# Kernel tuning notes

Measured on AMD Instinct MI355X. Metric: run time of the kernel, lower is better.

The kernel has to match this reference:

```python
import jax, jax.numpy as jnp
import numpy as np

B, T, D, K, P = 32, 512, 80, 16, 64
LAMBDA_MU = 0.1
LAMBDA_L = 0.1
N_SUBJECTS = float(P)


def _make_chol(key, prefix, d):
    # Valid lower-triangular Cholesky factors with positive diagonal.
    a = jax.random.normal(key, prefix + (d, d), dtype=jnp.float32) * 0.05
    strict = jnp.tril(a, -1)
    diag = 0.5 + jax.nn.softplus(jnp.einsum('...ii->...i', a))
    return strict + diag[..., None] * jnp.eye(d, dtype=jnp.float32)


def setup_inputs() -> dict:
    key = jax.random.key(0)
    k = jax.random.split(key, 7)
    x = jax.random.normal(k[0], (B, T, D), dtype=jnp.float32)
    g = jax.random.uniform(k[1], (B, T, K), dtype=jnp.float32)
    gamma = g / jnp.sum(g, axis=-1, keepdims=True)  # responsibilities sum to 1
    mu_pop = jax.random.normal(k[2], (K, D), dtype=jnp.float32) * 0.5
    mu_subj = mu_pop[None] + jax.random.normal(k[3], (P, K, D), dtype=jnp.float32) * 0.1
    L_pop = _make_chol(k[4], (K,), D)
    L_subj = _make_chol(k[5], (P, K), D)
    subject_ids = jax.random.randint(k[6], (B,), 0, P, dtype=jnp.int32)
    return dict(x=x, mu_pop=mu_pop, L_pop=L_pop, mu_subj=mu_subj,
                L_subj=L_subj, gamma=gamma, subject_ids=subject_ids)


def reference(x, mu_pop, L_pop, mu_subj, L_subj, gamma, subject_ids):
    dtype = mu_pop.dtype
    Bx, Tx, Dx = x.shape
    Pn = mu_subj.shape[0]
    # Gather subject parameters per batch row (equivalent to the TF
    # sort-by-subject + ragged per-block loop, vectorized).
    mu_b = mu_subj[subject_ids]   # (B,K,D)
    L_b = L_subj[subject_ids]     # (B,K,D,D)
    r = x[:, :, None, :] - mu_b[:, None, :, :]   # (B,T,K,D)
    rT = jnp.transpose(r, (0, 2, 3, 1))          # (B,K,D,T)
    y = jax.lax.linalg.triangular_solve(L_b, rT, left_side=True, lower=True)  # (B,K,D,T)
    mahal = jnp.sum(y * y, axis=2)               # (B,K,T)
    logdet = 2.0 * jnp.sum(jnp.log(jnp.diagonal(L_b, axis1=-2, axis2=-1)), axis=-1)  # (B,K)
    log2pi = jnp.asarray(np.log(2.0 * np.pi), dtype)
    logp = -0.5 * (Dx * log2pi + logdet[:, :, None] + mahal)  # (B,K,T)
    nll = -jnp.sum(jnp.transpose(gamma, (0, 2, 1)) * logp) / (Bx * Tx)
    # Regularization over subjects present in the batch.
    mask = jnp.zeros((Pn,), dtype).at[subject_ids].set(1.0)
    S = jnp.sum(mask)
    mu_reg = jnp.sum(mask[:, None, None] * jnp.square(mu_subj - mu_pop[None]))
    L_reg = jnp.sum(mask[:, None, None, None] * jnp.square(L_subj - L_pop[None]))
    scale = S / N_SUBJECTS
    return nll + scale * (LAMBDA_MU / 2.0 * mu_reg + LAMBDA_L / 2.0 * L_reg)
```

## Files before the change

kernel.cpp:

```cpp
#include <hip/hip_runtime.h>

#define NB 32
#define NT 512
#define ND 80
#define NK 16
#define NP 64

#define C_DLOG2PI (80.0f * 1.837877066409345f)

#define REG_CHUNKS 16

__global__ void zero_out_kernel(float* out) { out[0] = 0.0f; }

__global__ __launch_bounds__(512) void nll_kernel(
    const float* __restrict__ x,
    const float* __restrict__ mu_subj,
    const float* __restrict__ L_subj,
    const float* __restrict__ gamma,
    const int* __restrict__ sids,
    float* __restrict__ out)
{
    const int bk  = blockIdx.x;
    const int b   = bk / NK;
    const int k   = bk % NK;
    const int tid = threadIdx.x;
    const int s   = sids[b];

    __shared__ float Ls[ND * ND];
    __shared__ float mus[ND];
    __shared__ float invd[ND];
    __shared__ float logd[ND];
    __shared__ float logdet_sh;
    __shared__ float partial[8];

    const float* Lg = L_subj + (((size_t)s * NK + k) * ND * ND);
    for (int i = tid; i < ND * ND; i += 512) Ls[i] = Lg[i];
    const float* mg = mu_subj + (((size_t)s * NK + k) * ND);
    if (tid < ND) mus[tid] = mg[tid];
    __syncthreads();

    if (tid < ND) {
        float dg = Ls[tid * ND + tid];
        invd[tid] = 1.0f / dg;
        logd[tid] = logf(dg);
    }
    __syncthreads();
    if (tid == 0) {
        float sum = 0.0f;
        for (int i = 0; i < ND; ++i) sum += logd[i];
        logdet_sh = 2.0f * sum;
    }
    __syncthreads();
    const float logdet = logdet_sh;

    const int t = tid;
    const float* xp = x + (((size_t)b * NT + t) * ND);
    float r[ND];
    #pragma unroll
    for (int i4 = 0; i4 < ND / 4; ++i4) {
        float4 v = reinterpret_cast<const float4*>(xp)[i4];
        r[4 * i4 + 0] = v.x - mus[4 * i4 + 0];
        r[4 * i4 + 1] = v.y - mus[4 * i4 + 1];
        r[4 * i4 + 2] = v.z - mus[4 * i4 + 2];
        r[4 * i4 + 3] = v.w - mus[4 * i4 + 3];
    }

    float mahal = 0.0f;
    #pragma unroll
    for (int i = 0; i < ND; ++i) {
        float acc = r[i];
        #pragma unroll
        for (int j = 0; j < i; ++j) acc -= Ls[i * ND + j] * r[j];
        float yi = acc * invd[i];
        r[i] = yi;
        mahal += yi * yi;
    }

    float logp = -0.5f * (C_DLOG2PI + logdet + mahal);
    float g = gamma[(((size_t)b * NT + t) * NK) + k];
    float local = g * logp;

    #pragma unroll
    for (int off = 32; off > 0; off >>= 1) local += __shfl_down(local, off);
    int wave = tid >> 6;
    if ((tid & 63) == 0) partial[wave] = local;
    __syncthreads();
    if (tid == 0) {
        float sum = 0.0f;
        #pragma unroll
        for (int w = 0; w < 8; ++w) sum += partial[w];
        atomicAdd(out, -sum * (1.0f / (NB * NT)));
    }
}

__global__ __launch_bounds__(256) void reg_kernel(
    const float* __restrict__ mu_pop,
    const float* __restrict__ L_pop,
    const float* __restrict__ mu_subj,
    const float* __restrict__ L_subj,
    const int* __restrict__ sids,
    float* __restrict__ out)
{
    const int p   = blockIdx.y;
    const int c   = blockIdx.x;
    const int tid = threadIdx.x;

    __shared__ float scale_sh;
    __shared__ int   present_sh;
    __shared__ float partial[4];

    if (tid == 0) {
        unsigned long long seen = 0ull;
        int present = 0;
        for (int b = 0; b < NB; ++b) {
            int sb = sids[b];
            seen |= (1ull << sb);
            present |= (sb == p) ? 1 : 0;
        }
        present_sh = present;
        scale_sh = (float)__popcll(seen) * (1.0f / (float)NP);
    }
    __syncthreads();
    if (!present_sh) return;

    float acc = 0.0f;

    {
        const float4* Ls4 = reinterpret_cast<const float4*>(L_subj + (size_t)p * NK * ND * ND);
        const float4* Lp4 = reinterpret_cast<const float4*>(L_pop);
        const int n4 = NK * ND * ND / 4;
        for (int i = c * 256 + tid; i < n4; i += REG_CHUNKS * 256) {
            float4 a = Ls4[i];
            float4 bq = Lp4[i];
            float dx = a.x - bq.x, dy = a.y - bq.y, dz = a.z - bq.z, dw = a.w - bq.w;
            acc += dx * dx + dy * dy + dz * dz + dw * dw;
        }
    }
    if (c == 0) {
        const float4* ms4 = reinterpret_cast<const float4*>(mu_subj + (size_t)p * NK * ND);
        const float4* mp4 = reinterpret_cast<const float4*>(mu_pop);
        const int n4 = NK * ND / 4;
        for (int i = tid; i < n4; i += 256) {
            float4 a = ms4[i];
            float4 bq = mp4[i];
            float dx = a.x - bq.x, dy = a.y - bq.y, dz = a.z - bq.z, dw = a.w - bq.w;
            acc += dx * dx + dy * dy + dz * dz + dw * dw;
        }
    }

    #pragma unroll
    for (int off = 32; off > 0; off >>= 1) acc += __shfl_down(acc, off);
    int wave = tid >> 6;
    if ((tid & 63) == 0) partial[wave] = acc;
    __syncthreads();
    if (tid == 0) {
        float total = partial[0] + partial[1] + partial[2] + partial[3];
        atomicAdd(out, scale_sh * 0.05f * total);
    }
}

extern "C" void kernel_launch(void* const* d_in, const int* in_sizes, int n_in,
                              void* d_out, int out_size, void* d_ws, size_t ws_size,
                              hipStream_t stream) {
    (void)in_sizes; (void)n_in; (void)d_ws; (void)ws_size; (void)out_size;
    const float* x       = (const float*)d_in[0];
    const float* mu_pop  = (const float*)d_in[1];
    const float* L_pop   = (const float*)d_in[2];
    const float* mu_subj = (const float*)d_in[3];
    const float* L_subj  = (const float*)d_in[4];
    const float* gamma   = (const float*)d_in[5];
    const int*   sids    = (const int*)d_in[6];
    float* out = (float*)d_out;

    hipLaunchKernelGGL(zero_out_kernel, dim3(1), dim3(1), 0, stream, out);
    hipLaunchKernelGGL(nll_kernel, dim3(NB * NK), dim3(512), 0, stream,
                       x, mu_subj, L_subj, gamma, sids, out);
    hipLaunchKernelGGL(reg_kernel, dim3(REG_CHUNKS, NP), dim3(256), 0, stream,
                       mu_pop, L_pop, mu_subj, L_subj, sids, out);
}
```

Before: 69.98 us.

## Replace per-token triangular solve with explicit L inverse and bf16 MFMA GEMM

A new kernel inverts each selected Cholesky factor once per (batch, component) by forward substitution, stores L^-1 in bf16 in the workspace, and computes logdet. A second kernel then forms the residuals in bf16 and multiplies them by L^-1 with MFMA 16x16x32 bf16 instructions to get the Mahalanobis distances. This replaces the serial per-thread substitution that reads shared memory. It adds a kernel launch and workspace traffic, and bf16 rounding of the residuals and of L^-1 lowers accuracy.

```diff
diff --git a/kernel.cpp b/kernel.cpp
--- a/kernel.cpp
+++ b/kernel.cpp
@@ -9,87 +9,181 @@
 #define C_DLOG2PI (80.0f * 1.837877066409345f)
 
 #define REG_CHUNKS 16
+#define APAD 88
+
+typedef __attribute__((ext_vector_type(8))) short bf16x8;
+typedef __attribute__((ext_vector_type(4))) short s16x4;
+typedef __attribute__((ext_vector_type(4))) float f32x4;
+
+__device__ inline unsigned short f2bf(float f) {
+    unsigned u = __float_as_uint(f);
+    unsigned r = (u + 0x7fffu + ((u >> 16) & 1u)) >> 16;
+    return (unsigned short)r;
+}
 
 __global__ void zero_out_kernel(float* out) { out[0] = 0.0f; }
 
-__global__ __launch_bounds__(512) void nll_kernel(
+__global__ __launch_bounds__(128, 1) void inv_kernel(
+    const float* __restrict__ L_subj,
+    const int* __restrict__ sids,
+    unsigned short* __restrict__ linv_ws,
+    float* __restrict__ logdet_ws)
+{
+    const int bk = blockIdx.x;
+    const int b  = bk >> 4;
+    const int k  = bk & 15;
+    const int c  = threadIdx.x;
+    const int s  = __builtin_amdgcn_readfirstlane(sids[b]);
+    const float* __restrict__ Lg = L_subj + (((size_t)s * NK + k) * ND * ND);
+
+    __shared__ unsigned short T_sh[ND * APAD];
+
+    float v[ND];
+    float logdet = 0.0f;
+    #pragma unroll
+    for (int i = 0; i < ND; ++i) {
+        const float* Lrow = Lg + i * ND;
+        float acc = (i == c) ? 1.0f : 0.0f;
+        #pragma unroll
+        for (int j = 0; j < i; ++j) acc -= Lrow[j] * v[j];
+        float d = Lrow[i];
+        v[i] = acc / d;
+        logdet += logf(d);
+    }
+
+    if (c < ND) {
+        #pragma unroll
+        for (int i = 0; i < ND; ++i) T_sh[i * APAD + c] = f2bf(v[i]);
+    }
+    if (c == 0) logdet_ws[bk] = 2.0f * logdet;
+    __syncthreads();
+
+    uint4* dst = (uint4*)(linv_ws + (size_t)bk * (ND * ND));
+    for (int i = threadIdx.x; i < ND * ND / 8; i += 128) {
+        int n  = i / 10;
+        int c8 = (i % 10) * 8;
+        dst[i] = *(const uint4*)&T_sh[n * APAD + c8];
+    }
+}
+
+__global__ __launch_bounds__(256) void gemm_kernel(
     const float* __restrict__ x,
     const float* __restrict__ mu_subj,
-    const float* __restrict__ L_subj,
     const float* __restrict__ gamma,
     const int* __restrict__ sids,
+    const unsigned short* __restrict__ linv_ws,
+    const float* __restrict__ logdet_ws,
     float* __restrict__ out)
 {
-    const int bk  = blockIdx.x;
-    const int b   = bk / NK;
-    const int k   = bk % NK;
-    const int tid = threadIdx.x;
-    const int s   = sids[b];
-
-    __shared__ float Ls[ND * ND];
-    __shared__ float mus[ND];
-    __shared__ float invd[ND];
-    __shared__ float logd[ND];
-    __shared__ float logdet_sh;
-    __shared__ float partial[8];
-
-    const float* Lg = L_subj + (((size_t)s * NK + k) * ND * ND);
-    for (int i = tid; i < ND * ND; i += 512) Ls[i] = Lg[i];
-    const float* mg = mu_subj + (((size_t)s * NK + k) * ND);
-    if (tid < ND) mus[tid] = mg[tid];
-    __syncthreads();
-
-    if (tid < ND) {
-        float dg = Ls[tid * ND + tid];
-        invd[tid] = 1.0f / dg;
-        logd[tid] = logf(dg);
-    }
+    const int bx = blockIdx.x;
+    const int k  = bx & 15;
+    const int tt = (bx >> 4) & 3;
+    const int b  = bx >> 6;
+    const int bk = b * NK + k;
+    const int t0 = tt * 128;
+    const int tid  = threadIdx.x;
+    const int lane = tid & 63;
+    const int wv   = tid >> 6;
+    const int m    = lane & 15;
+    const int g    = lane >> 4;
+    const int s    = __builtin_amdgcn_readfirstlane(sids[b]);
+
+    __shared__ unsigned short A_sh[128 * APAD];
+    __shared__ unsigned short B_sh[ND * APAD];
+
+    {
+        const int r = tid >> 1;
+        const int h = tid & 1;
+        const float4* xp = (const float4*)(x + ((size_t)(b * NT + t0 + r)) * ND + h * 40);
+        const float4* mp = (const float4*)(mu_subj + ((size_t)(s * NK + k)) * ND + h * 40);
+        #pragma unroll
+        for (int q = 0; q < 10; ++q) {
+            float4 xv = xp[q];
+            float4 mv = mp[q];
+            s16x4 pk;
+            pk.x = (short)f2bf(xv.x - mv.x);
+            pk.y = (short)f2bf(xv.y - mv.y);
+            pk.z = (short)f2bf(xv.z - mv.z);
+            pk.w = (short)f2bf(xv.w - mv.w);
+            *(s16x4*)&A_sh[r * APAD + h * 40 + q * 4] = pk;
+        }
+    }
+    {
+        const uint4* src = (const uint4*)(linv_ws + (size_t)bk * (ND * ND));
+        for (int i = tid; i < ND * ND / 8; i += 256) {
+            int n  = i / 10;
+            int c8 = (i % 10) * 8;
+            *(uint4*)&B_sh[n * APAD + c8] = src[i];
+        }
+    }
+    __syncthreads();
+
+    f32x4 acc[2][5];
+    #pragma unroll
+    for (int mt = 0; mt < 2; ++mt)
+        #pragma unroll
+        for (int nt = 0; nt < 5; ++nt)
+            acc[mt][nt] = (f32x4){0.f, 0.f, 0.f, 0.f};
+
+    const bf16x8 zf = {0, 0, 0, 0, 0, 0, 0, 0};
+    #pragma unroll
+    for (int ks = 0; ks < 3; ++ks) {
+        const int kbase = ks * 32 + g * 8;
+        bf16x8 af[2], bfr[5];
+        if (kbase < ND) {
+            af[0] = *(const bf16x8*)&A_sh[(wv * 32 + m) * APAD + kbase];
+            af[1] = *(const bf16x8*)&A_sh[(wv * 32 + 16 + m) * APAD + kbase];
+            #pragma unroll
+            for (int nt = 0; nt < 5; ++nt)
+                bfr[nt] = *(const bf16x8*)&B_sh[(nt * 16 + m) * APAD + kbase];
+        } else {
+            af[0] = zf; af[1] = zf;
+            #pragma unroll
+            for (int nt = 0; nt < 5; ++nt) bfr[nt] = zf;
+        }
+        #pragma unroll
+        for (int mt = 0; mt < 2; ++mt)
+            #pragma unroll
+            for (int nt = 0; nt < 5; ++nt)
+                acc[mt][nt] = __builtin_amdgcn_mfma_f32_16x16x32_bf16(
+                    af[mt], bfr[nt], acc[mt][nt], 0, 0, 0);
+    }
+
+    const float ldet_c = logdet_ws[bk] + C_DLOG2PI;
+    float local = 0.0f;
+    #pragma unroll
+    for (int mt = 0; mt < 2; ++mt) {
+        float p0 = 0.f, p1 = 0.f, p2 = 0.f, p3 = 0.f;
+        #pragma unroll
+        for (int nt = 0; nt < 5; ++nt) {
+            p0 += acc[mt][nt][0] * acc[mt][nt][0];
+            p1 += acc[mt][nt][1] * acc[mt][nt][1];
+            p2 += acc[mt][nt][2] * acc[mt][nt][2];
+            p3 += acc[mt][nt][3] * acc[mt][nt][3];
+        }
+        #pragma unroll
+        for (int mask = 1; mask < 16; mask <<= 1) {
+            p0 += __shfl_xor(p0, mask);
+            p1 += __shfl_xor(p1, mask);
+            p2 += __shfl_xor(p2, mask);
+            p3 += __shfl_xor(p3, mask);
+        }
+        if (m < 4) {
+            float mm = (m == 0) ? p0 : (m == 1) ? p1 : (m == 2) ? p2 : p3;
+            int t = t0 + wv * 32 + mt * 16 + g * 4 + m;
+            float gam = gamma[((size_t)(b * NT + t)) * NK + k];
+            local += gam * (mm + ldet_c);
+        }
+    }
+
+    __shared__ float partial[4];
+    #pragma unroll
+    for (int off = 32; off > 0; off >>= 1) local += __shfl_down(local, off);
+    if (lane == 0) partial[wv] = local;
     __syncthreads();
     if (tid == 0) {
-        float sum = 0.0f;
-        for (int i = 0; i < ND; ++i) sum += logd[i];
-        logdet_sh = 2.0f * sum;
-    }
-    __syncthreads();
-    const float logdet = logdet_sh;
-
-    const int t = tid;
-    const float* xp = x + (((size_t)b * NT + t) * ND);
-    float r[ND];
-    #pragma unroll
-    for (int i4 = 0; i4 < ND / 4; ++i4) {
-        float4 v = reinterpret_cast<const float4*>(xp)[i4];
-        r[4 * i4 + 0] = v.x - mus[4 * i4 + 0];
-        r[4 * i4 + 1] = v.y - mus[4 * i4 + 1];
-        r[4 * i4 + 2] = v.z - mus[4 * i4 + 2];
-        r[4 * i4 + 3] = v.w - mus[4 * i4 + 3];
-    }
-
-    float mahal = 0.0f;
-    #pragma unroll
-    for (int i = 0; i < ND; ++i) {
-        float acc = r[i];
-        #pragma unroll
-        for (int j = 0; j < i; ++j) acc -= Ls[i * ND + j] * r[j];
-        float yi = acc * invd[i];
-        r[i] = yi;
-        mahal += yi * yi;
-    }
-
-    float logp = -0.5f * (C_DLOG2PI + logdet + mahal);
-    float g = gamma[(((size_t)b * NT + t) * NK) + k];
-    float local = g * logp;
-
-    #pragma unroll
-    for (int off = 32; off > 0; off >>= 1) local += __shfl_down(local, off);
-    int wave = tid >> 6;
-    if ((tid & 63) == 0) partial[wave] = local;
-    __syncthreads();
-    if (tid == 0) {
-        float sum = 0.0f;
-        #pragma unroll
-        for (int w = 0; w < 8; ++w) sum += partial[w];
-        atomicAdd(out, -sum * (1.0f / (NB * NT)));
+        float sum = partial[0] + partial[1] + partial[2] + partial[3];
+        atomicAdd(out, sum * (0.5f / (NB * NT)));
     }
 }
 
@@ -124,7 +218,6 @@
     if (!present_sh) return;
 
     float acc = 0.0f;
-
     {
         const float4* Ls4 = reinterpret_cast<const float4*>(L_subj + (size_t)p * NK * ND * ND);
         const float4* Lp4 = reinterpret_cast<const float4*>(L_pop);
@@ -162,7 +255,7 @@
 extern "C" void kernel_launch(void* const* d_in, const int* in_sizes, int n_in,
                               void* d_out, int out_size, void* d_ws, size_t ws_size,
                               hipStream_t stream) {
-    (void)in_sizes; (void)n_in; (void)d_ws; (void)ws_size; (void)out_size;
+    (void)in_sizes; (void)n_in; (void)ws_size; (void)out_size;
     const float* x       = (const float*)d_in[0];
     const float* mu_pop  = (const float*)d_in[1];
     const float* L_pop   = (const float*)d_in[2];
@@ -172,9 +265,14 @@
     const int*   sids    = (const int*)d_in[6];
     float* out = (float*)d_out;
 
+    unsigned short* linv_ws = (unsigned short*)d_ws;
+    float* logdet_ws = (float*)((char*)d_ws + (size_t)NB * NK * ND * ND * 2);
+
     hipLaunchKernelGGL(zero_out_kernel, dim3(1), dim3(1), 0, stream, out);
-    hipLaunchKernelGGL(nll_kernel, dim3(NB * NK), dim3(512), 0, stream,
-                       x, mu_subj, L_subj, gamma, sids, out);
+    hipLaunchKernelGGL(inv_kernel, dim3(NB * NK), dim3(128), 0, stream,
+                       L_subj, sids, linv_ws, logdet_ws);
+    hipLaunchKernelGGL(gemm_kernel, dim3(NB * 4 * NK), dim3(256), 0, stream,
+                       x, mu_subj, gamma, sids, linv_ws, logdet_ws, out);
     hipLaunchKernelGGL(reg_kernel, dim3(REG_CHUNKS, NP), dim3(256), 0, stream,
                        mu_pop, L_pop, mu_subj, L_subj, sids, out);
 }
```

New measurement: 123.5 us. 1.77x slower.
